# Performance work log

Hardware: AMD Instinct MI355X
Metric: run time of the kernel (lower is better)

The kernel has to match this reference:

```python
import jax, jax.numpy as jnp
import numpy as np

K = 4096
D = 64
DECAY = 0.99
EPS = 1e-05


def setup_inputs() -> dict:
    key = jax.random.key(0)
    k1, k2 = jax.random.split(key)
    z_e = jax.random.normal(k1, (32, 1024, D), dtype=jnp.float32)
    emb = jax.random.normal(k2, (K, D), dtype=jnp.float32)
    emb = emb / jnp.clip(jnp.linalg.norm(emb, axis=1, keepdims=True), 1e-8)
    return {
        "z_e": z_e,
        "embedding": emb,
        "ema_cluster_size": jnp.zeros((K,), jnp.float32),
        "ema_embedding": jnp.zeros((K, D), jnp.float32),
    }


def reference(z_e, embedding, ema_cluster_size, ema_embedding):
    B, L, Dd = z_e.shape
    flat = z_e.reshape(-1, Dd)                                   # (N, D)
    flat_norm = flat / jnp.clip(jnp.linalg.norm(flat, axis=1, keepdims=True), 1e-8)
    dots = flat_norm @ embedding.T                               # (N, K)
    indices = jnp.argmax(dots, axis=1)                           # (N,)
    z_q = embedding[indices].reshape(B, L, Dd)
    z_q_st = z_e + jax.lax.stop_gradient(z_q - z_e)

    # ---- usage / stats ----
    usage = jnp.zeros((K,), jnp.float32).at[indices].add(1.0)    # bincount
    probs = usage / jnp.maximum(usage.sum(), 1.0)
    safe = jnp.where(probs > 0, probs, 1.0)
    perplexity = jnp.exp(-jnp.sum(probs * jnp.log(safe)))
    dead_ratio = jnp.mean((usage == 0).astype(jnp.float32))
    stats = jnp.stack([perplexity, dead_ratio])

    # ---- EMA update (training-mode buffer math, functional) ----
    fn = jax.lax.stop_gradient(flat_norm)
    embed_sum = jnp.zeros((K, Dd), jnp.float32).at[indices].add(fn)  # one_hot.T @ flat_norm
    new_cs = DECAY * ema_cluster_size + (1.0 - DECAY) * usage
    new_ema_emb = DECAY * ema_embedding + (1.0 - DECAY) * embed_sum
    n = new_cs.sum()
    smoothed = (new_cs + EPS) / (n + K * EPS)
    norm_e = new_ema_emb / jnp.clip(smoothed, EPS)[:, None]
    norm_e = norm_e / jnp.clip(jnp.linalg.norm(norm_e, axis=1, keepdims=True), 1e-8)

    # ---- dead-code reinit (reinit_prob=1.0, threshold=0); deterministic key ----
    N = fn.shape[0]
    rand_idx = jax.random.randint(jax.random.key(1), (K,), 0, N)
    src = fn[rand_idx]
    src = src / jnp.clip(jnp.linalg.norm(src, axis=1, keepdims=True), 1e-8)
    dead = usage <= 0.0
    new_embedding = jnp.where(dead[:, None], src, norm_e)

    return (z_q_st, z_q, indices.reshape(B, L), stats,
            new_embedding, new_cs, new_ema_emb)
```

## Files before the change

### kernel.cpp

```cpp
#include <hip/hip_runtime.h>
#include <math.h>

#define N_TOK 32768
#define KCB   4096
#define SPLITS 6

#define OFF_ZQST   0
#define OFF_ZQ     2097152
#define OFF_IDX    4194304
#define OFF_STATS  4227072
#define OFF_NEWEMB 4227074
#define OFF_NEWCS  4489218
#define OFF_NEWEMA 4493314

#define WS_FN       0
#define WS_ESUM     8388608
#define WS_USAGE    9437184
#define WS_CNTS     9453568
#define WS_FULLKEY  9454592
#define WS_EHI      9716736
#define WS_ELO      10241024
#define WS_PK1      10765312
#define WS_PK2      11551744
#define WS_IDXW     12338176
#define WS_RIDX     12469248
#define WS_FULL     12485632

#define THRKEY 131072u
#define DGRKEY 98304u

typedef __attribute__((ext_vector_type(8))) short short8;
typedef __attribute__((ext_vector_type(4))) float float4v;

__device__ __forceinline__ float wave_sum(float v) {
#pragma unroll
  for (int off = 32; off > 0; off >>= 1) v += __shfl_xor(v, off, 64);
  return v;
}

__device__ __forceinline__ unsigned short f2bf(float f) {
  unsigned u = __float_as_uint(f);
  unsigned r = (u + 0x7fffu + ((u >> 16) & 1u)) >> 16;
  return (unsigned short)r;
}
__device__ __forceinline__ float bf2f(unsigned short h) {
  return __uint_as_float(((unsigned)h) << 16);
}

__device__ __forceinline__ unsigned rotl32(unsigned x, int d) {
  return (x << d) | (x >> (32 - d));
}
__device__ __forceinline__ void tf2x32(unsigned k0, unsigned k1,
                                       unsigned x0, unsigned x1,
                                       unsigned& o0, unsigned& o1) {
  unsigned ks2 = k0 ^ k1 ^ 0x1BD11BDAu;
  unsigned v0 = x0 + k0, v1 = x1 + k1;
  v0 += v1; v1 = rotl32(v1, 13) ^ v0;
  v0 += v1; v1 = rotl32(v1, 15) ^ v0;
  v0 += v1; v1 = rotl32(v1, 26) ^ v0;
  v0 += v1; v1 = rotl32(v1, 6) ^ v0;
  v0 += k1; v1 += ks2 + 1u;
  v0 += v1; v1 = rotl32(v1, 17) ^ v0;
  v0 += v1; v1 = rotl32(v1, 29) ^ v0;
  v0 += v1; v1 = rotl32(v1, 16) ^ v0;
  v0 += v1; v1 = rotl32(v1, 24) ^ v0;
  v0 += ks2; v1 += k0 + 2u;
  v0 += v1; v1 = rotl32(v1, 13) ^ v0;
  v0 += v1; v1 = rotl32(v1, 15) ^ v0;
  v0 += v1; v1 = rotl32(v1, 26) ^ v0;
  v0 += v1; v1 = rotl32(v1, 6) ^ v0;
  v0 += k0; v1 += k1 + 3u;
  v0 += v1; v1 = rotl32(v1, 17) ^ v0;
  v0 += v1; v1 = rotl32(v1, 29) ^ v0;
  v0 += v1; v1 = rotl32(v1, 16) ^ v0;
  v0 += v1; v1 = rotl32(v1, 24) ^ v0;
  v0 += k1; v1 += ks2 + 4u;
  v0 += v1; v1 = rotl32(v1, 13) ^ v0;
  v0 += v1; v1 = rotl32(v1, 15) ^ v0;
  v0 += v1; v1 = rotl32(v1, 26) ^ v0;
  v0 += v1; v1 = rotl32(v1, 6) ^ v0;
  v0 += ks2; v1 += k0 + 5u;
  o0 = v0; o1 = v1;
}

__global__ __launch_bounds__(256) void k_prep(const float* __restrict__ z_e,
                                              const float* __restrict__ emb,
                                              float* __restrict__ fn,
                                              unsigned short* __restrict__ ehi,
                                              unsigned short* __restrict__ elo,
                                              int* __restrict__ ridx,
                                              int* __restrict__ zbase) {
  int b = blockIdx.x;
  int t = threadIdx.x;
  if (b < 8192) {
    int n = b * 4 + (t >> 6);
    int lane = t & 63;
    float x = z_e[n * 64 + lane];
    float ss = wave_sum(x * x);
    fn[n * 64 + lane] = x / fmaxf(sqrtf(ss), 1e-8f);
  } else if (b < 9216) {
    int i = (b - 8192) * 256 + t;
    float x = emb[i];
    unsigned short h = f2bf(x);
    ehi[i] = h;
    elo[i] = f2bf(x - bf2f(h));
  } else if (b < 9224) {
    int j = (b - 9216) * 256 + t;
    unsigned a0, b0, a1, b1;
    tf2x32(0u, 1u, 0u, 2u, a0, b0);
    tf2x32(0u, 1u, 1u, 3u, a1, b1);
    unsigned o0, o1;
    tf2x32(b0, b1, (unsigned)j, (unsigned)(j + 2048), o0, o1);
    ridx[j] = (int)(o0 & 32767u);
    ridx[j + 2048] = (int)(o1 & 32767u);
  } else {
    int i = (b - 9224) * 256 + t;
    zbase[i] = 0;
  }
}

__global__ __launch_bounds__(256, 3) void k_dots(const float* __restrict__ fn,
                                                 const unsigned short* __restrict__ ehi,
                                                 const unsigned short* __restrict__ elo,
                                                 unsigned* __restrict__ pk1,
                                                 unsigned* __restrict__ pk2) {
  int t = threadIdx.x;
  int wave = t >> 6, lane = t & 63;
  int g = lane >> 4, n = lane & 15;
  int qw = blockIdx.x * 256 + wave * 64;
  int split = blockIdx.y;
  int nt16 = (split < 2) ? 704 : 672;
  int tstart16 = (split < 3) ? 704 * split : 672 * split + 64;
  int ntiles = nt16 >> 4;

  short8 ahi[4][2], alo[4][2];
#pragma unroll
  for (int s = 0; s < 4; s++)
#pragma unroll
    for (int ks = 0; ks < 2; ks++) {
      const float* src = fn + (qw + s * 16 + n) * 64 + ks * 32 + g * 8;
      short8 h, l;
#pragma unroll
      for (int j = 0; j < 8; j++) {
        float f = src[j] * 0.25f;
        unsigned short hu = f2bf(f);
        h[j] = (short)hu;
        l[j] = (short)f2bf(f - bf2f(hu));
      }
      ahi[s][ks] = h;
      alo[s][ks] = l;
    }

  unsigned run1[4][4], run2[4][4];
#pragma unroll
  for (int s = 0; s < 4; s++)
#pragma unroll
    for (int r = 0; r < 4; r++) { run1[s][r] = 0u; run2[s][r] = 0u; }

  const unsigned short* bh = ehi + (tstart16 + n) * 64 + g * 8;
  const unsigned short* bl = elo + (tstart16 + n) * 64 + g * 8;
  const float hiclamp = __uint_as_float(0x3F9FFFFFu);

  short8 h0a = *(const short8*)(bh);
  short8 h1a = *(const short8*)(bh + 32);
  short8 l0a = *(const short8*)(bl);
  short8 l1a = *(const short8*)(bl + 32);
  short8 h0b = *(const short8*)(bh + 1024);
  short8 h1b = *(const short8*)(bh + 1024 + 32);
  short8 l0b = *(const short8*)(bl + 1024);
  short8 l1b = *(const short8*)(bl + 1024 + 32);

#define MFMA_BLOCK(H0, H1, L0, L1)                                              \
    float4v a0 = (float4v){1.125f, 1.125f, 1.125f, 1.125f};                     \
    float4v a1 = a0, a2 = a0, a3 = a0;                                          \
    a0 = __builtin_amdgcn_mfma_f32_16x16x32_bf16(alo[0][0], H0, a0, 0, 0, 0);   \
    a1 = __builtin_amdgcn_mfma_f32_16x16x32_bf16(alo[1][0], H0, a1, 0, 0, 0);   \
    a2 = __builtin_amdgcn_mfma_f32_16x16x32_bf16(alo[2][0], H0, a2, 0, 0, 0);   \
    a3 = __builtin_amdgcn_mfma_f32_16x16x32_bf16(alo[3][0], H0, a3, 0, 0, 0);   \
    a0 = __builtin_amdgcn_mfma_f32_16x16x32_bf16(alo[0][1], H1, a0, 0, 0, 0);   \
    a1 = __builtin_amdgcn_mfma_f32_16x16x32_bf16(alo[1][1], H1, a1, 0, 0, 0);   \
    a2 = __builtin_amdgcn_mfma_f32_16x16x32_bf16(alo[2][1], H1, a2, 0, 0, 0);   \
    a3 = __builtin_amdgcn_mfma_f32_16x16x32_bf16(alo[3][1], H1, a3, 0, 0, 0);   \
    a0 = __builtin_amdgcn_mfma_f32_16x16x32_bf16(ahi[0][0], L0, a0, 0, 0, 0);   \
    a1 = __builtin_amdgcn_mfma_f32_16x16x32_bf16(ahi[1][0], L0, a1, 0, 0, 0);   \
    a2 = __builtin_amdgcn_mfma_f32_16x16x32_bf16(ahi[2][0], L0, a2, 0, 0, 0);   \
    a3 = __builtin_amdgcn_mfma_f32_16x16x32_bf16(ahi[3][0], L0, a3, 0, 0, 0);   \
    a0 = __builtin_amdgcn_mfma_f32_16x16x32_bf16(ahi[0][1], L1, a0, 0, 0, 0);   \
    a1 = __builtin_amdgcn_mfma_f32_16x16x32_bf16(ahi[1][1], L1, a1, 0, 0, 0);   \
    a2 = __builtin_amdgcn_mfma_f32_16x16x32_bf16(ahi[2][1], L1, a2, 0, 0, 0);   \
    a3 = __builtin_amdgcn_mfma_f32_16x16x32_bf16(ahi[3][1], L1, a3, 0, 0, 0);   \
    a0 = __builtin_amdgcn_mfma_f32_16x16x32_bf16(ahi[0][0], H0, a0, 0, 0, 0);   \
    a1 = __builtin_amdgcn_mfma_f32_16x16x32_bf16(ahi[1][0], H0, a1, 0, 0, 0);   \
    a2 = __builtin_amdgcn_mfma_f32_16x16x32_bf16(ahi[2][0], H0, a2, 0, 0, 0);   \
    a3 = __builtin_amdgcn_mfma_f32_16x16x32_bf16(ahi[3][0], H0, a3, 0, 0, 0);   \
    a0 = __builtin_amdgcn_mfma_f32_16x16x32_bf16(ahi[0][1], H1, a0, 0, 0, 0);   \
    a1 = __builtin_amdgcn_mfma_f32_16x16x32_bf16(ahi[1][1], H1, a1, 0, 0, 0);   \
    a2 = __builtin_amdgcn_mfma_f32_16x16x32_bf16(ahi[2][1], H1, a2, 0, 0, 0);   \
    a3 = __builtin_amdgcn_mfma_f32_16x16x32_bf16(ahi[3][1], H1, a3, 0, 0, 0);

#define SELECT_BLOCK(KT)                                                        \
    {                                                                           \
      unsigned invb = (unsigned)(nt16 - 1 - (KT) * 16 - n);                     \
      _Pragma("unroll") for (int r = 0; r < 4; r++) {                           \
        float x0 = __builtin_amdgcn_fmed3f(a0[r], 1.0f, hiclamp);               \
        unsigned kb0 = (__float_as_uint(x0) << 10) + invb;                      \
        run2[0][r] = max(run2[0][r], min(run1[0][r], kb0));                     \
        run1[0][r] = max(run1[0][r], kb0);                                      \
        float x1 = __builtin_amdgcn_fmed3f(a1[r], 1.0f, hiclamp);               \
        unsigned kb1 = (__float_as_uint(x1) << 10) + invb;                      \
        run2[1][r] = max(run2[1][r], min(run1[1][r], kb1));                     \
        run1[1][r] = max(run1[1][r], kb1);                                      \
        float x2 = __builtin_amdgcn_fmed3f(a2[r], 1.0f, hiclamp);               \
        unsigned kb2 = (__float_as_uint(x2) << 10) + invb;                      \
        run2[2][r] = max(run2[2][r], min(run1[2][r], kb2));                     \
        run1[2][r] = max(run1[2][r], kb2);                                      \
        float x3 = __builtin_amdgcn_fmed3f(a3[r], 1.0f, hiclamp);               \
        unsigned kb3 = (__float_as_uint(x3) << 10) + invb;                      \
        run2[3][r] = max(run2[3][r], min(run1[3][r], kb3));                     \
        run1[3][r] = max(run1[3][r], kb3);                                      \
      }                                                                         \
    }

#pragma unroll 1
  for (int kt = 0; kt < ntiles; kt += 2) {
    {
      MFMA_BLOCK(h0a, h1a, l0a, l1a)
      int off = (kt + 2) * 1024;
      h0a = *(const short8*)(bh + off);
      h1a = *(const short8*)(bh + off + 32);
      l0a = *(const short8*)(bl + off);
      l1a = *(const short8*)(bl + off + 32);
      SELECT_BLOCK(kt)
    }
    {
      MFMA_BLOCK(h0b, h1b, l0b, l1b)
      int off = (kt + 3) * 1024;
      h0b = *(const short8*)(bh + off);
      h1b = *(const short8*)(bh + off + 32);
      l0b = *(const short8*)(bl + off);
      l1b = *(const short8*)(bl + off + 32);
      SELECT_BLOCK(kt + 1)
    }
  }
#undef MFMA_BLOCK
#undef SELECT_BLOCK

#pragma unroll
  for (int off = 1; off <= 8; off <<= 1) {
#pragma unroll
    for (int s = 0; s < 4; s++)
#pragma unroll
      for (int r = 0; r < 4; r++) {
        unsigned o1 = (unsigned)__shfl_xor((int)run1[s][r], off, 64);
        unsigned o2 = (unsigned)__shfl_xor((int)run2[s][r], off, 64);
        run2[s][r] = max(min(run1[s][r], o1), max(run2[s][r], o2));
        run1[s][r] = max(run1[s][r], o1);
      }
  }

  if (n == 0) {
#pragma unroll
    for (int s = 0; s < 4; s++)
#pragma unroll
      for (int r = 0; r < 4; r++) {
        int q = qw + s * 16 + g * 4 + r;
        pk1[split * N_TOK + q] = run1[s][r];
        pk2[split * N_TOK + q] = run2[s][r];
      }
  }
}

__global__ __launch_bounds__(256) void k_merge_fix(const unsigned* __restrict__ pk1,
                                                   const unsigned* __restrict__ pk2,
                                                   const float* __restrict__ fn,
                                                   const float* __restrict__ emb,
                                                   int* __restrict__ idxw,
                                                   int* __restrict__ cnts,
                                                   int* __restrict__ full,
                                                   unsigned long long* __restrict__ fullkey) {
  __shared__ int nfl;
  __shared__ int fl[256][13];
  int t = threadIdx.x;
  if (t == 0) nfl = 0;
  __syncthreads();
  int q = blockIdx.x * 256 + t;
  unsigned k1v[SPLITS], k2v[SPLITS];
  unsigned b1 = 0u, b2 = 0u;
  int s1 = 0;
#pragma unroll
  for (int s = 0; s < SPLITS; s++) {
    unsigned k1 = pk1[s * N_TOK + q];
    unsigned k2 = pk2[s * N_TOK + q];
    k1v[s] = k1;
    k2v[s] = k2;
    b2 = max(b2, min(b1, k1));
    b2 = max(b2, k2);
    if (k1 > b1) { b1 = k1; s1 = s; }
  }
  int nt16s = (s1 < 2) ? 704 : 672;
  int ts16 = (s1 < 3) ? 704 * s1 : 672 * s1 + 64;
  idxw[q] = ts16 + nt16s - 1 - (int)(b1 & 1023u);
  fullkey[q] = 0ull;
  bool danger = false;
#pragma unroll
  for (int s = 0; s < SPLITS; s++) danger |= (k2v[s] + DGRKEY > b1);
  if (danger) {
    int p = atomicAdd(&cnts[0], 1);
    full[p] = q;
  } else if (b1 - b2 < THRKEY) {
    int p = atomicAdd(&nfl, 1);
    fl[p][0] = q;
#pragma unroll
    for (int s = 0; s < SPLITS; s++) {
      int nt = (s < 2) ? 704 : 672;
      int tss = (s < 3) ? 704 * s : 672 * s + 64;
      fl[p][1 + s] = tss + nt - 1 - (int)(k1v[s] & 1023u);
      fl[p][7 + s] = tss + nt - 1 - (int)(k2v[s] & 1023u);
    }
  }
  __syncthreads();
  int m = nfl;
  int wave = t >> 6, lane = t & 63;
  int c = lane >> 2, dg = lane & 3;
  for (int i = wave; i < m; i += 4) {
    int fq = fl[i][0];
    int code = (c < 12) ? fl[i][1 + c] : fl[i][1];
    const float* er = emb + code * 64 + dg * 16;
    const float* fr = fn + fq * 64 + dg * 16;
    double d = 0.0;
#pragma unroll
    for (int k = 0; k < 16; k++) d += (double)er[k] * (double)fr[k];
    d += __shfl_xor(d, 1, 64);
    d += __shfl_xor(d, 2, 64);
    unsigned long long key =
        ((unsigned long long)__double_as_longlong(d + 2.0) & ~0xFFFULL) |
        (unsigned long long)(4095 - code);
    if (c >= 12) key = 0ull;
#pragma unroll
    for (int off = 4; off <= 32; off <<= 1) {
      unsigned long long o = __shfl_xor(key, off, 64);
      key = key > o ? key : o;
    }
    if (lane == 0) idxw[fq] = 4095 - (int)(key & 0xFFFULL);
  }
}

__global__ __launch_bounds__(256) void k_fix_full(const int* __restrict__ cnts,
                                                  const int* __restrict__ full,
                                                  const float* __restrict__ fn,
                                                  const float* __restrict__ emb,
                                                  unsigned long long* __restrict__ fullkey) {
  __shared__ float sfn[64];
  __shared__ unsigned long long red[256];
  int t = threadIdx.x;
  int chunk = blockIdx.x & 15;
  int c = chunk * 256 + t;
  float cr[64];
  {
    const float4v* er4 = (const float4v*)(emb + c * 64);
#pragma unroll
    for (int kk = 0; kk < 16; kk++) {
      float4v v = er4[kk];
      cr[kk * 4 + 0] = v[0];
      cr[kk * 4 + 1] = v[1];
      cr[kk * 4 + 2] = v[2];
      cr[kk * 4 + 3] = v[3];
    }
  }
  int total = cnts[0];
  total = total < N_TOK ? total : N_TOK;
  int qstride = (int)(gridDim.x >> 4);
  for (int w = (int)(blockIdx.x >> 4); w < total; w += qstride) {
    int q = full[w];
    __syncthreads();
    if (t < 64) sfn[t] = fn[q * 64 + t];
    __syncthreads();
    double s0 = 0, s1 = 0, s2 = 0, s3 = 0;
#pragma unroll
    for (int k = 0; k < 16; k++) {
      s0 += (double)cr[k] * (double)sfn[k];
      s1 += (double)cr[k + 16] * (double)sfn[k + 16];
      s2 += (double)cr[k + 32] * (double)sfn[k + 32];
      s3 += (double)cr[k + 48] * (double)sfn[k + 48];
    }
    double d = (s0 + s1) + (s2 + s3);
    unsigned long long key =
        ((unsigned long long)__double_as_longlong(d + 2.0) & ~0xFFFULL) |
        (unsigned long long)(4095 - c);
    red[t] = key;
    __syncthreads();
    for (int s = 128; s > 0; s >>= 1) {
      if (t < s) red[t] = red[t] > red[t + s] ? red[t] : red[t + s];
      __syncthreads();
    }
    if (t == 0) atomicMax(&fullkey[q], red[0]);
  }
}

__global__ __launch_bounds__(256) void k_write_scatter(const int* __restrict__ idxw,
                                                       const unsigned long long* __restrict__ fullkey,
                                                       const float* __restrict__ z_e,
                                                       const float* __restrict__ emb,
                                                       const float* __restrict__ fn,
                                                       float* __restrict__ out,
                                                       float* __restrict__ esum,
                                                       float* __restrict__ usage) {
  int t = threadIdx.x;
  int nn = blockIdx.x * 4 + (t >> 6);
  int lane = t & 63;
  unsigned long long fk = fullkey[nn];
  int bi = fk ? (4095 - (int)(fk & 0xFFFULL)) : idxw[nn];
  float v = emb[bi * 64 + lane];
  float ze = z_e[nn * 64 + lane];
  out[OFF_ZQST + nn * 64 + lane] = ze + (v - ze);
  out[OFF_ZQ + nn * 64 + lane] = v;
  atomicAdd(&esum[bi * 64 + lane], fn[nn * 64 + lane]);
  if (lane == 0) {
    out[OFF_IDX + nn] = (float)bi;
    atomicAdd(&usage[bi], 1.0f);
  }
}

__global__ __launch_bounds__(256) void k_stats(const float* __restrict__ usage,
                                               const float* __restrict__ ema_cs,
                                               float* __restrict__ scal) {
  __shared__ float rE[4], rD[4], rC[4];
  int t = threadIdx.x;
  int i = blockIdx.x * 256 + t;
  float u = usage[i];
  float p = u * (1.0f / 32768.0f);
  float ent = (p > 0.f) ? p * logf(p) : 0.f;
  float dead = (u == 0.f) ? 1.f : 0.f;
  float cs = 0.99f * ema_cs[i] + 0.01f * u;
  ent = wave_sum(ent);
  dead = wave_sum(dead);
  cs = wave_sum(cs);
  int w = t >> 6, lane = t & 63;
  if (lane == 0) { rE[w] = ent; rD[w] = dead; rC[w] = cs; }
  __syncthreads();
  if (t == 0) {
    atomicAdd(&scal[0], rE[0] + rE[1] + rE[2] + rE[3]);
    atomicAdd(&scal[1], rD[0] + rD[1] + rD[2] + rD[3]);
    atomicAdd(&scal[2], rC[0] + rC[1] + rC[2] + rC[3]);
  }
}

__global__ __launch_bounds__(256) void k_final(const float* __restrict__ usage,
                                               const float* __restrict__ ema_cs,
                                               const float* __restrict__ ema_emb,
                                               const float* __restrict__ esum,
                                               const float* __restrict__ fn,
                                               const int* __restrict__ ridx,
                                               const float* __restrict__ scal,
                                               float* __restrict__ out) {
  int t = threadIdx.x;
  int k = blockIdx.x * 4 + (t >> 6);
  int lane = t & 63;
  if (blockIdx.x == 0 && t == 0) {
    out[OFF_STATS + 0] = expf(-scal[0]);
    out[OFF_STATS + 1] = scal[1] * (1.0f / 4096.0f);
  }
  float u = usage[k];
  float ncs = 0.99f * ema_cs[k] + 0.01f * u;
  if (lane == 0) out[OFF_NEWCS + k] = ncs;
  float nee = 0.99f * ema_emb[k * 64 + lane] + 0.01f * esum[k * 64 + lane];
  out[OFF_NEWEMA + k * 64 + lane] = nee;

  float n = scal[2];
  float smoothed = (ncs + 1e-5f) / (n + 4096.0f * 1e-5f);
  float ne = nee / fmaxf(smoothed, 1e-5f);
  float ss = wave_sum(ne * ne);
  ne = ne / fmaxf(sqrtf(ss), 1e-8f);

  float res;
  if (u <= 0.f) {
    int rsrc = ridx[k];
    float v = fn[rsrc * 64 + lane];
    float s2 = wave_sum(v * v);
    res = v / fmaxf(sqrtf(s2), 1e-8f);
  } else {
    res = ne;
  }
  out[OFF_NEWEMB + k * 64 + lane] = res;
}

extern "C" void kernel_launch(void* const* d_in, const int* in_sizes, int n_in,
                              void* d_out, int out_size, void* d_ws, size_t ws_size,
                              hipStream_t stream) {
  const float* z_e = (const float*)d_in[0];
  const float* emb = (const float*)d_in[1];
  const float* ema_cs = (const float*)d_in[2];
  const float* ema_emb = (const float*)d_in[3];
  float* out = (float*)d_out;
  char* ws = (char*)d_ws;

  float* fn = (float*)(ws + WS_FN);
  float* esum = (float*)(ws + WS_ESUM);
  float* usage = (float*)(ws + WS_USAGE);
  int* cnts = (int*)(ws + WS_CNTS);
  float* scal = (float*)(ws + WS_CNTS + 16);
  unsigned long long* fullkey = (unsigned long long*)(ws + WS_FULLKEY);
  unsigned short* ehi = (unsigned short*)(ws + WS_EHI);
  unsigned short* elo = (unsigned short*)(ws + WS_ELO);
  unsigned* pk1 = (unsigned*)(ws + WS_PK1);
  unsigned* pk2 = (unsigned*)(ws + WS_PK2);
  int* idxw = (int*)(ws + WS_IDXW);
  int* ridx = (int*)(ws + WS_RIDX);
  int* full = (int*)(ws + WS_FULL);

  k_prep<<<10265, 256, 0, stream>>>(z_e, emb, fn, ehi, elo, ridx, (int*)(ws + WS_ESUM));
  k_dots<<<dim3(128, SPLITS), 256, 0, stream>>>(fn, ehi, elo, pk1, pk2);
  k_merge_fix<<<128, 256, 0, stream>>>(pk1, pk2, fn, emb, idxw, cnts, full, fullkey);
  k_fix_full<<<1024, 256, 0, stream>>>(cnts, full, fn, emb, fullkey);
  k_write_scatter<<<8192, 256, 0, stream>>>(idxw, fullkey, z_e, emb, fn, out, esum, usage);
  k_stats<<<16, 256, 0, stream>>>(usage, ema_cs, scal);
  k_final<<<1024, 256, 0, stream>>>(usage, ema_cs, ema_emb, esum, fn, ridx, scal, out);
}
```

Before: 174.2 us.

## Stage codebook tiles into LDS via async global_load_lds double buffering

In the dots kernel, each wave previously loaded its own copy of the bf16 hi/lo codebook tiles directly from global memory into registers. Now the four waves of a block cooperatively copy each pair of tiles into a double-buffered, XOR-swizzled shared-memory buffer with global_load_lds, and each wave reads its fragments from there. This removes redundant global and L2 traffic across waves and overlaps the next copy with the current MFMA work. In exchange it adds a block barrier per tile pair, 16KB of LDS per block, and depends on the swizzle matching the MFMA operand layout.

```diff
diff --git a/kernel.cpp b/kernel.cpp
--- a/kernel.cpp
+++ b/kernel.cpp
@@ -45,6 +45,12 @@
 }
 __device__ __forceinline__ float bf2f(unsigned short h) {
   return __uint_as_float(((unsigned)h) << 16);
+}
+
+typedef const __attribute__((address_space(1))) unsigned int* gas_ptr;
+typedef __attribute__((address_space(3))) unsigned int* las_ptr;
+__device__ __forceinline__ void gl_lds16(const void* g, void* l) {
+  __builtin_amdgcn_global_load_lds((gas_ptr)g, (las_ptr)l, 16, 0, 0);
 }
 
 __device__ __forceinline__ unsigned rotl32(unsigned x, int d) {
@@ -124,6 +130,7 @@
                                                  const unsigned short* __restrict__ elo,
                                                  unsigned* __restrict__ pk1,
                                                  unsigned* __restrict__ pk2) {
+  __shared__ unsigned short lds_b[2][2][2][1024];
   int t = threadIdx.x;
   int wave = t >> 6, lane = t & 63;
   int g = lane >> 4, n = lane & 15;
@@ -132,6 +139,7 @@
   int nt16 = (split < 2) ? 704 : 672;
   int tstart16 = (split < 3) ? 704 * split : 672 * split + 64;
   int ntiles = nt16 >> 4;
+  int npairs = ntiles >> 1;
 
   short8 ahi[4][2], alo[4][2];
 #pragma unroll
@@ -157,18 +165,23 @@
 #pragma unroll
     for (int r = 0; r < 4; r++) { run1[s][r] = 0u; run2[s][r] = 0u; }
 
-  const unsigned short* bh = ehi + (tstart16 + n) * 64 + g * 8;
-  const unsigned short* bl = elo + (tstart16 + n) * 64 + g * 8;
   const float hiclamp = __uint_as_float(0x3F9FFFFFu);
 
-  short8 h0a = *(const short8*)(bh);
-  short8 h1a = *(const short8*)(bh + 32);
-  short8 l0a = *(const short8*)(bl);
-  short8 l1a = *(const short8*)(bl + 32);
-  short8 h0b = *(const short8*)(bh + 1024);
-  short8 h1b = *(const short8*)(bh + 1024 + 32);
-  short8 l0b = *(const short8*)(bl + 1024);
-  short8 l1b = *(const short8*)(bl + 1024 + 32);
+  int stile = wave >> 1;
+  int shl = wave & 1;
+  const unsigned short* sbase = shl ? elo : ehi;
+  int c0 = lane ^ ((lane >> 3) & 7);
+
+#define STAGE(BUF, PAIR)                                                        \
+    {                                                                           \
+      const unsigned short* sg =                                                \
+          sbase + (tstart16 + ((PAIR) * 2 + stile) * 16) * 64;                  \
+      gl_lds16(sg + c0 * 8, &lds_b[BUF][stile][shl][0]);                        \
+      gl_lds16(sg + 512 + c0 * 8, &lds_b[BUF][stile][shl][512]);                \
+    }
+
+  int sh0 = (n * 8 + (g ^ (n & 7))) * 8;
+  int sh1 = (n * 8 + ((g + 4) ^ (n & 7))) * 8;
 
 #define MFMA_BLOCK(H0, H1, L0, L1)                                              \
     float4v a0 = (float4v){1.125f, 1.125f, 1.125f, 1.125f};                     \
@@ -221,29 +234,34 @@
       }                                                                         \
     }
 
+  STAGE(0, 0)
+  __syncthreads();
+  int bb = 0;
 #pragma unroll 1
-  for (int kt = 0; kt < ntiles; kt += 2) {
+  for (int p = 0; p < npairs; p++) {
+    if (p + 1 < npairs) STAGE(bb ^ 1, p + 1)
     {
-      MFMA_BLOCK(h0a, h1a, l0a, l1a)
-      int off = (kt + 2) * 1024;
-      h0a = *(const short8*)(bh + off);
-      h1a = *(const short8*)(bh + off + 32);
-      l0a = *(const short8*)(bl + off);
-      l1a = *(const short8*)(bl + off + 32);
-      SELECT_BLOCK(kt)
+      short8 H0 = *(const short8*)&lds_b[bb][0][0][sh0];
+      short8 H1 = *(const short8*)&lds_b[bb][0][0][sh1];
+      short8 L0 = *(const short8*)&lds_b[bb][0][1][sh0];
+      short8 L1 = *(const short8*)&lds_b[bb][0][1][sh1];
+      MFMA_BLOCK(H0, H1, L0, L1)
+      SELECT_BLOCK(p * 2)
     }
     {
-      MFMA_BLOCK(h0b, h1b, l0b, l1b)
-      int off = (kt + 3) * 1024;
-      h0b = *(const short8*)(bh + off);
-      h1b = *(const short8*)(bh + off + 32);
-      l0b = *(const short8*)(bl + off);
-      l1b = *(const short8*)(bl + off + 32);
-      SELECT_BLOCK(kt + 1)
-    }
+      short8 H0 = *(const short8*)&lds_b[bb][1][0][sh0];
+      short8 H1 = *(const short8*)&lds_b[bb][1][0][sh1];
+      short8 L0 = *(const short8*)&lds_b[bb][1][1][sh0];
+      short8 L1 = *(const short8*)&lds_b[bb][1][1][sh1];
+      MFMA_BLOCK(H0, H1, L0, L1)
+      SELECT_BLOCK(p * 2 + 1)
+    }
+    __syncthreads();
+    bb ^= 1;
   }
 #undef MFMA_BLOCK
 #undef SELECT_BLOCK
+#undef STAGE
 
 #pragma unroll
   for (int off = 1; off <= 8; off <<= 1) {
```

After: 156.4 us. 1.11x faster.
